# Kernel tuning notes

Measured on AMD Instinct MI355X. Metric: run time of the kernel, lower is better.

## Reference

```python
import jax, jax.numpy as jnp
import numpy as np

DIM = 128
NH = 4
K = 7
PAD = K // 2  # dilation = 1
MLP_HID = 4 * DIM
EPS = 1e-5


def _layernorm(x, w, b):
    m = jnp.mean(x, axis=-1, keepdims=True)
    v = jnp.mean((x - m) ** 2, axis=-1, keepdims=True)
    return (x - m) / jnp.sqrt(v + EPS) * w + b


def _windows(xp, H, W):
    # xp: [B, nh, Hp, Wp, hd] zero-padded; returns [B, nh, H, W, hd, K*K]
    return jnp.stack(
        [xp[:, :, i:i + H, j:j + W, :] for i in range(K) for j in range(K)],
        axis=-1,
    )


def setup_inputs() -> dict:
    key = jax.random.key(0)
    ks = jax.random.split(key, 10)
    s = 0.02
    inp = {
        "x": jax.random.normal(ks[0], (4, 56, 56, DIM), dtype=jnp.float32),
        "ln1_w": jnp.ones((DIM,), jnp.float32),
        "ln1_b": jnp.zeros((DIM,), jnp.float32),
        "w_qkv": jax.random.normal(ks[1], (DIM, 3 * DIM), jnp.float32) * s,
        "b_qkv": jnp.zeros((3 * DIM,), jnp.float32),
        "rpb": jax.random.normal(ks[2], (NH, K * K), jnp.float32) * s,
        "w_proj": jax.random.normal(ks[3], (DIM, DIM), jnp.float32) * s,
        "b_proj": jnp.zeros((DIM,), jnp.float32),
        "ln2_w": jnp.ones((DIM,), jnp.float32),
        "ln2_b": jnp.zeros((DIM,), jnp.float32),
        "w_fc1": jax.random.normal(ks[4], (DIM, MLP_HID), jnp.float32) * s,
        "b_fc1": jnp.zeros((MLP_HID,), jnp.float32),
        "w_fc2": jax.random.normal(ks[5], (MLP_HID, DIM), jnp.float32) * s,
        "b_fc2": jnp.zeros((DIM,), jnp.float32),
    }
    return inp


def _nat_block(x, ln1_w, ln1_b, w_qkv, b_qkv, rpb, w_proj, b_proj,
               ln2_w, ln2_b, w_fc1, b_fc1, w_fc2, b_fc2):
    B, H, W, C = x.shape
    hd = C // NH
    scale = hd ** -0.5

    # --- neighborhood attention ---
    xn = _layernorm(x, ln1_w, ln1_b)
    qkv = xn @ w_qkv + b_qkv                       # [B,H,W,3C]
    qkv = qkv.reshape(B, H, W, 3, NH, hd)
    qkv = jnp.transpose(qkv, (3, 0, 4, 1, 2, 5))   # [3,B,nh,H,W,hd]
    q, k, v = qkv[0] * scale, qkv[1], qkv[2]
    # zero-pad spatial dims (matches F.pad with constant 0 in original)
    pad = ((0, 0), (0, 0), (PAD, PAD), (PAD, PAD), (0, 0))
    kp = jnp.pad(k, pad)
    vp = jnp.pad(v, pad)
    kw = _windows(kp, H, W)                        # [B,nh,H,W,hd,49]
    vw = _windows(vp, H, W)
    attn = jnp.einsum('bnhwd,bnhwdk->bnhwk', q, kw)
    attn = attn + rpb[None, :, None, None, :]
    attn = jax.nn.softmax(attn, axis=-1)
    out = jnp.einsum('bnhwk,bnhwdk->bnhwd', attn, vw)  # [B,nh,H,W,hd]
    out = jnp.transpose(out, (0, 2, 3, 1, 4)).reshape(B, H, W, C)
    x = x + (out @ w_proj + b_proj)

    # --- MLP ---
    xn2 = _layernorm(x, ln2_w, ln2_b)
    h = jax.nn.gelu(xn2 @ w_fc1 + b_fc1, approximate=False)
    x = x + (h @ w_fc2 + b_fc2)
    return x


def reference(x, ln1_w, ln1_b, w_qkv, b_qkv, rpb, w_proj, b_proj,
              ln2_w, ln2_b, w_fc1, b_fc1, w_fc2, b_fc2):
    return _nat_block(x, ln1_w, ln1_b, w_qkv, b_qkv, rpb, w_proj, b_proj,
                      ln2_w, ln2_b, w_fc1, b_fc1, w_fc2, b_fc2)
```

## Files before the change

### kernel.cpp

```cpp
#include <hip/hip_runtime.h>

using bf16x8 = __attribute__((ext_vector_type(8))) short;
using f32x4  = __attribute__((ext_vector_type(4))) float;
typedef unsigned short u16;
typedef __attribute__((ext_vector_type(8))) unsigned short u16x8;
typedef __attribute__((ext_vector_type(4))) unsigned short u16x4;

__device__ __forceinline__ u16 f2b(float f){
  unsigned int i=__float_as_uint(f);
  return (u16)((i + 0x7FFFu + ((i>>16)&1u))>>16);
}
__device__ __forceinline__ float b2f(u16 u){
  union{unsigned int i; float f;}v; v.i=((unsigned int)u)<<16; return v.f;
}
__device__ __forceinline__ void async16(const void* g, void* l){
  __builtin_amdgcn_global_load_lds((__attribute__((address_space(1))) void*)(g),
                                   (__attribute__((address_space(3))) void*)(l), 16, 0, 0);
}
__device__ __forceinline__ float gelu_tanh(float v){
  float u = v*(0.7978845608f + 0.0356774081f*v*v);
  float e = __expf(-2.0f*fabsf(u));
  float th = (1.0f-e)/(1.0f+e);
  th = (u<0.f)? -th : th;
  return 0.5f*v*(1.0f+th);
}

__global__ void prep_kernel(const float* __restrict__ wqkv, const float* __restrict__ wproj,
                            const float* __restrict__ wfc1, const float* __restrict__ wfc2,
                            u16* __restrict__ tqkv, u16* __restrict__ tproj,
                            u16* __restrict__ tfc1, u16* __restrict__ tfc2)
{
  int idx = blockIdx.x*256 + threadIdx.x;
  if (idx < 49152){ int n=idx>>7, k=idx&127; tqkv[idx]=f2b(wqkv[k*384+n]); }
  else if (idx < 65536){ int t=idx-49152; int n=t>>7, k=t&127; tproj[t]=f2b(wproj[k*128+n]); }
  else if (idx < 131072){ int t=idx-65536; int n=t>>7, k=t&127; tfc1[t]=f2b(wfc1[k*512+n]); }
  else if (idx < 196608){ int t=idx-131072; int n=t>>9, k=t&511; tfc2[t]=f2b(wfc2[k*128+n]); }
}

__global__ __launch_bounds__(256)
void qkv_ln_kernel(const float* __restrict__ x,
                   const float* __restrict__ ln1w, const float* __restrict__ ln1b,
                   const u16* __restrict__ tqkv, const float* __restrict__ bqkv,
                   u16* __restrict__ qb, u16* __restrict__ kb, u16* __restrict__ vb)
{
  __shared__ __align__(16) char smem[49152];
  char* lA = smem;
  char* lB = smem + 16384;

  const int tid = threadIdx.x;
  const int lane = tid&63, wid = tid>>6;
  const int quad = lane>>4, lrow = lane&15;
  const int m0 = blockIdx.x*64;
  const int wm = (wid&1)*32, wn = (wid>>1)*64;

  {
    const int row = tid>>2, q = tid&3;
    float xv[32];
    const float4* xr = (const float4*)(x + (size_t)(m0+row)*128 + q*32);
    float s=0.f, sq=0.f;
    #pragma unroll
    for (int c4=0;c4<8;c4++){
      float4 t = xr[c4];
      xv[c4*4]=t.x; xv[c4*4+1]=t.y; xv[c4*4+2]=t.z; xv[c4*4+3]=t.w;
      s += t.x+t.y+t.z+t.w;
      sq += t.x*t.x+t.y*t.y+t.z*t.z+t.w*t.w;
    }
    s  += __shfl_xor(s,1);  s  += __shfl_xor(s,2);
    sq += __shfl_xor(sq,1); sq += __shfl_xor(sq,2);
    float mean = s*0.0078125f;
    float rstd = rsqrtf(sq*0.0078125f - mean*mean + 1e-5f);
    const float4* wr = (const float4*)(ln1w + q*32);
    const float4* br = (const float4*)(ln1b + q*32);
    u16 nv[32];
    #pragma unroll
    for (int c4=0;c4<8;c4++){
      float4 w4 = wr[c4], b4 = br[c4];
      nv[c4*4]   = f2b((xv[c4*4]  -mean)*rstd*w4.x + b4.x);
      nv[c4*4+1] = f2b((xv[c4*4+1]-mean)*rstd*w4.y + b4.y);
      nv[c4*4+2] = f2b((xv[c4*4+2]-mean)*rstd*w4.z + b4.z);
      nv[c4*4+3] = f2b((xv[c4*4+3]-mean)*rstd*w4.w + b4.w);
    }
    #pragma unroll
    for (int cc=0;cc<4;cc++){
      u16x8 pk;
      #pragma unroll
      for (int e=0;e<8;e++) pk[e] = nv[cc*8+e];
      *(u16x8*)(lA + (((q*4+cc)*64 + row)<<4)) = pk;
    }
  }

  for (int nc=0; nc<3; nc++){
    __syncthreads();
    #pragma unroll
    for (int kk=0;kk<8;kk++){
      int i = tid + kk*256;
      int n = i&127, c = i>>7;
      async16(tqkv + (size_t)(nc*128+n)*128 + c*8, lB + i*16);
    }
    __syncthreads();

    f32x4 acc[2][4] = {};
    #pragma unroll
    for (int ks=0;ks<4;ks++){
      bf16x8 af[2], bfr[4];
      #pragma unroll
      for (int i=0;i<2;i++) af[i]  = ((const bf16x8*)lA)[(ks*4+quad)*64  + wm + i*16 + lrow];
      #pragma unroll
      for (int j=0;j<4;j++) bfr[j] = ((const bf16x8*)lB)[(ks*4+quad)*128 + wn + j*16 + lrow];
      #pragma unroll
      for (int i=0;i<2;i++)
        #pragma unroll
        for (int j=0;j<4;j++)
          acc[i][j] = __builtin_amdgcn_mfma_f32_16x16x32_bf16(af[i], bfr[j], acc[i][j], 0,0,0);
    }

    const float scale = 0.17677669529663687f;
    u16* dst = (nc==0)? qb : ((nc==1)? kb : vb);
    #pragma unroll
    for (int j=0;j<4;j++){
      int col = wn + j*16 + lrow;
      float bia = bqkv[nc*128 + col];
      #pragma unroll
      for (int i=0;i<2;i++){
        #pragma unroll
        for (int r=0;r<4;r++){
          int row = m0 + wm + i*16 + quad*4 + r;
          float val = acc[i][j][r] + bia;
          if (nc==0) val *= scale;
          dst[(size_t)row*128 + col] = f2b(val);
        }
      }
    }
  }
}

#define KT_S 40
#define VT_S 232
#define P_S  152
__global__ __launch_bounds__(256)
void attn_kernel(const u16* __restrict__ qb, const u16* __restrict__ kb,
                 const u16* __restrict__ vb, const float* __restrict__ rpb,
                 u16* __restrict__ aout)
{
  __shared__ __align__(16) char smem[50192];
  u16*  kt   = (u16*)smem;
  u16*  vt   = (u16*)(smem + 15680);
  u16*  Pm   = (u16*)(smem + 30528);
  float* srpb= (float*)(smem + 49984);

  const int tid = threadIdx.x;
  const int tile = blockIdx.x, bh = blockIdx.y;
  const int b = bh>>2, h = bh&3;
  const int ty = (tile/7)*8, tx = (tile%7)*8;
  const int lane = tid&63, wid = tid>>6;
  const int quad = lane>>4, lrow = lane&15;

  #pragma unroll
  for (int kk=0;kk<4;kk++){
    int i = tid + kk*256;
    if (i < 784){
      int pos = i>>2, oct = i&3;
      int hy = pos/14, hx = pos - hy*14;
      int gy = ty + hy - 3, gx = tx + hx - 3;
      u16x8 kv = {0,0,0,0,0,0,0,0};
      if (gy>=0 && gy<56 && gx>=0 && gx<56)
        kv = *(const u16x8*)(kb + ((size_t)(b*3136 + gy*56 + gx)*128 + h*32 + oct*8));
      *(u16x8*)(kt + pos*KT_S + oct*8) = kv;
    }
  }
  #pragma unroll
  for (int kk=0;kk<4;kk++){
    int i = tid + kk*256;
    if (i < 896){
      int pos = i>>2, oct = i&3;
      u16x8 vv = {0,0,0,0,0,0,0,0};
      if (pos < 196){
        int hy = pos/14, hx = pos - hy*14;
        int gy = ty + hy - 3, gx = tx + hx - 3;
        if (gy>=0 && gy<56 && gx>=0 && gx<56)
          vv = *(const u16x8*)(vb + ((size_t)(b*3136 + gy*56 + gx)*128 + h*32 + oct*8));
      }
      #pragma unroll
      for (int j=0;j<8;j++) vt[(oct*8+j)*VT_S + pos] = vv[j];
    }
  }
  if (tid < 49) srpb[tid] = rpb[h*49 + tid];
  __syncthreads();

  const int pxq = wid*16 + lrow;
  const int tokq = b*3136 + (ty + (pxq>>3))*56 + tx + (pxq&7);
  bf16x8 qf = *(const bf16x8*)(qb + (size_t)tokq*128 + h*32 + quad*8);

  f32x4 sc[7];
  const f32x4 zf = {0.f,0.f,0.f,0.f};
  #pragma unroll
  for (int cg=0;cg<7;cg++){
    int pos = wid*28 + cg*16 + lrow;
    bf16x8 kf = *(const bf16x8*)(kt + pos*KT_S + quad*8);
    sc[cg] = __builtin_amdgcn_mfma_f32_16x16x32_bf16(qf, kf, zf, 0,0,0);
  }

  const int lyq = quad>>1;
  #pragma unroll
  for (int cg=0;cg<7;cg++){
    int np = cg*16 + lrow;
    int nh = np/14, hx = np - nh*14;
    int dy = nh - lyq;
    #pragma unroll
    for (int r=0;r<4;r++){
      int lx = (quad*4+r)&7;
      int dx = hx - lx;
      bool in = ((unsigned)dy<7u) && ((unsigned)dx<7u);
      float bias = srpb[in ? (dy*7+dx) : 0];
      sc[cg][r] = in ? (sc[cg][r] + bias) : -1e30f;
    }
  }
  float rmax[4], lsum[4], inv[4];
  #pragma unroll
  for (int r=0;r<4;r++){
    float m = sc[0][r];
    #pragma unroll
    for (int cg=1;cg<7;cg++) m = fmaxf(m, sc[cg][r]);
    m = fmaxf(m, __shfl_xor(m,1)); m = fmaxf(m, __shfl_xor(m,2));
    m = fmaxf(m, __shfl_xor(m,4)); m = fmaxf(m, __shfl_xor(m,8));
    rmax[r] = m;
    float l = 0.f;
    #pragma unroll
    for (int cg=0;cg<7;cg++){ float p = __expf(sc[cg][r]-m); sc[cg][r]=p; l+=p; }
    l += __shfl_xor(l,1); l += __shfl_xor(l,2);
    l += __shfl_xor(l,4); l += __shfl_xor(l,8);
    lsum[r]=l; inv[r]=1.f/l;
  }

  u16* Pw = Pm + wid*16*P_S;
  #pragma unroll
  for (int cg=0;cg<7;cg++){
    int np = cg*16 + lrow;
    #pragma unroll
    for (int r=0;r<4;r++)
      Pw[(quad*4+r)*P_S + np] = f2b(sc[cg][r]);
  }
  { int zr = lane>>2, seg = lane&3;
    u16x4 z4 = {0,0,0,0};
    *(u16x4*)(Pw + zr*P_S + 112 + seg*4) = z4; }
  __syncthreads();

  f32x4 oacc[2] = {zf, zf};
  #pragma unroll
  for (int ks=0;ks<4;ks++){
    bf16x8 pf = *(const bf16x8*)(Pw + lrow*P_S + ks*32 + quad*8);
    #pragma unroll
    for (int cg2=0;cg2<2;cg2++){
      bf16x8 vf = *(const bf16x8*)(vt + (cg2*16+lrow)*VT_S + wid*28 + ks*32 + quad*8);
      oacc[cg2] = __builtin_amdgcn_mfma_f32_16x16x32_bf16(pf, vf, oacc[cg2], 0,0,0);
    }
  }
  #pragma unroll
  for (int r=0;r<4;r++){
    int px = wid*16 + quad*4 + r;
    int tok = b*3136 + (ty + (px>>3))*56 + tx + (px&7);
    #pragma unroll
    for (int cg2=0;cg2<2;cg2++){
      int ch = cg2*16 + lrow;
      aout[(size_t)tok*128 + h*32 + ch] = f2b(oacc[cg2][r]*inv[r]);
    }
  }
}

__global__ __launch_bounds__(256)
void mega_mlp_kernel(const u16* __restrict__ aout, const float* __restrict__ x,
                     const u16* __restrict__ tproj, const float* __restrict__ bproj,
                     const float* __restrict__ ln2w, const float* __restrict__ ln2b,
                     const u16* __restrict__ tfc1, const float* __restrict__ bfc1,
                     const u16* __restrict__ tfc2, const float* __restrict__ bfc2,
                     float* __restrict__ out)
{
  __shared__ __align__(16) char smem[65536];
  char* lA  = smem;
  char* lB  = smem + 16384;
  char* xn2 = smem + 49152;

  const int tid = threadIdx.x;
  const int lane = tid&63, wid = tid>>6;
  const int quad = lane>>4, lrow = lane&15;
  const int m0 = blockIdx.x*64;
  const int wm = (wid&1)*32, wn = (wid>>1)*64;
  const int half = wid>>1;

  #pragma unroll
  for (int kk=0;kk<4;kk++){
    int i = tid + kk*256;
    int row = i&63, c = i>>6;
    async16(aout + (size_t)(m0+row)*128 + c*8, lA + i*16);
  }
  #pragma unroll
  for (int kk=0;kk<8;kk++){
    int i = tid + kk*256;
    int n = i&127, c = i>>7;
    async16(tproj + (size_t)n*128 + c*8, lB + i*16);
  }
  __syncthreads();

  f32x4 acc[2][4] = {};
  #pragma unroll
  for (int ks=0;ks<4;ks++){
    bf16x8 af[2], bfr[4];
    #pragma unroll
    for (int i=0;i<2;i++) af[i]  = ((const bf16x8*)lA)[(ks*4+quad)*64  + wm + i*16 + lrow];
    #pragma unroll
    for (int j=0;j<4;j++) bfr[j] = ((const bf16x8*)lB)[(ks*4+quad)*128 + wn + j*16 + lrow];
    #pragma unroll
    for (int i=0;i<2;i++)
      #pragma unroll
      for (int j=0;j<4;j++)
        acc[i][j] = __builtin_amdgcn_mfma_f32_16x16x32_bf16(af[i], bfr[j], acc[i][j], 0,0,0);
  }
  __syncthreads();

  float x1v[2][4][4];
  float ps[2][4] = {}, pq[2][4] = {};
  #pragma unroll
  for (int j=0;j<4;j++){
    int col = wn + j*16 + lrow;
    float bia = bproj[col];
    #pragma unroll
    for (int i=0;i<2;i++){
      #pragma unroll
      for (int r=0;r<4;r++){
        int row = m0 + wm + i*16 + quad*4 + r;
        float val = acc[i][j][r] + bia + x[(size_t)row*128 + col];
        x1v[i][j][r] = val;
        ps[i][r] += val; pq[i][r] += val*val;
      }
    }
  }
  #pragma unroll
  for (int i=0;i<2;i++)
    #pragma unroll
    for (int r=0;r<4;r++){
      #pragma unroll
      for (int off=1; off<16; off<<=1){
        ps[i][r] += __shfl_xor(ps[i][r], off);
        pq[i][r] += __shfl_xor(pq[i][r], off);
      }
    }
  float* redS = (float*)lA;
  float* redQ = redS + 128;
  if (lrow==0){
    #pragma unroll
    for (int i=0;i<2;i++)
      #pragma unroll
      for (int r=0;r<4;r++){
        int row = wm + i*16 + quad*4 + r;
        redS[half*64 + row] = ps[i][r];
        redQ[half*64 + row] = pq[i][r];
      }
  }
  __syncthreads();

  {
    float w2[4], b2[4];
    #pragma unroll
    for (int j=0;j<4;j++){ int col = wn+j*16+lrow; w2[j]=ln2w[col]; b2[j]=ln2b[col]; }
    #pragma unroll
    for (int i=0;i<2;i++){
      #pragma unroll
      for (int r=0;r<4;r++){
        int row = wm + i*16 + quad*4 + r;
        float mean = (redS[row] + redS[64+row])*0.0078125f;
        float var  = (redQ[row] + redQ[64+row])*0.0078125f - mean*mean;
        float rstd = rsqrtf(var + 1e-5f);
        #pragma unroll
        for (int j=0;j<4;j++){
          int col = wn + j*16 + lrow;
          u16 hv = f2b((x1v[i][j][r]-mean)*rstd*w2[j] + b2[j]);
          ((u16*)xn2)[((col>>3)*64 + row)*8 + (col&7)] = hv;
        }
      }
    }
  }
  __syncthreads();

  f32x4 acc3[2][4] = {};
  for (int nc=0; nc<4; nc++){
    if (nc>0) __syncthreads();
    #pragma unroll
    for (int kk=0;kk<8;kk++){
      int i = tid + kk*256;
      int n = i&127, c = i>>7;
      async16(tfc1 + (size_t)(nc*128+n)*128 + c*8, lB + i*16);
    }
    __syncthreads();

    f32x4 acc2[2][4] = {};
    #pragma unroll
    for (int ks=0;ks<4;ks++){
      bf16x8 af[2], bfr[4];
      #pragma unroll
      for (int i=0;i<2;i++) af[i]  = ((const bf16x8*)xn2)[(ks*4+quad)*64  + wm + i*16 + lrow];
      #pragma unroll
      for (int j=0;j<4;j++) bfr[j] = ((const bf16x8*)lB)[(ks*4+quad)*128 + wn + j*16 + lrow];
      #pragma unroll
      for (int i=0;i<2;i++)
        #pragma unroll
        for (int j=0;j<4;j++)
          acc2[i][j] = __builtin_amdgcn_mfma_f32_16x16x32_bf16(af[i], bfr[j], acc2[i][j], 0,0,0);
    }
    #pragma unroll
    for (int j=0;j<4;j++){
      int col = wn + j*16 + lrow;
      float bia = bfc1[nc*128 + col];
      #pragma unroll
      for (int i=0;i<2;i++){
        #pragma unroll
        for (int r=0;r<4;r++){
          int row = wm + i*16 + quad*4 + r;
          float g = gelu_tanh(acc2[i][j][r] + bia);
          ((u16*)lA)[((col>>3)*64 + row)*8 + (col&7)] = f2b(g);
        }
      }
    }
    __syncthreads();
    #pragma unroll
    for (int kk=0;kk<8;kk++){
      int i = tid + kk*256;
      int n = i&127, c = i>>7;
      async16(tfc2 + (size_t)n*512 + nc*128 + c*8, lB + i*16);
    }
    __syncthreads();

    #pragma unroll
    for (int ks=0;ks<4;ks++){
      bf16x8 af[2], bfr[4];
      #pragma unroll
      for (int i=0;i<2;i++) af[i]  = ((const bf16x8*)lA)[(ks*4+quad)*64  + wm + i*16 + lrow];
      #pragma unroll
      for (int j=0;j<4;j++) bfr[j] = ((const bf16x8*)lB)[(ks*4+quad)*128 + wn + j*16 + lrow];
      #pragma unroll
      for (int i=0;i<2;i++)
        #pragma unroll
        for (int j=0;j<4;j++)
          acc3[i][j] = __builtin_amdgcn_mfma_f32_16x16x32_bf16(af[i], bfr[j], acc3[i][j], 0,0,0);
    }
  }

  #pragma unroll
  for (int j=0;j<4;j++){
    int col = wn + j*16 + lrow;
    float bia = bfc2[col];
    #pragma unroll
    for (int i=0;i<2;i++){
      #pragma unroll
      for (int r=0;r<4;r++){
        int row = m0 + wm + i*16 + quad*4 + r;
        out[(size_t)row*128 + col] = acc3[i][j][r] + bia + x1v[i][j][r];
      }
    }
  }
}

extern "C" void kernel_launch(void* const* d_in, const int* in_sizes, int n_in,
                              void* d_out, int out_size, void* d_ws, size_t ws_size,
                              hipStream_t stream)
{
  const float* x     =(const float*)d_in[0];
  const float* ln1w  =(const float*)d_in[1];
  const float* ln1b  =(const float*)d_in[2];
  const float* wqkv  =(const float*)d_in[3];
  const float* bqkv  =(const float*)d_in[4];
  const float* rpb   =(const float*)d_in[5];
  const float* wproj =(const float*)d_in[6];
  const float* bproj =(const float*)d_in[7];
  const float* ln2w  =(const float*)d_in[8];
  const float* ln2b  =(const float*)d_in[9];
  const float* wfc1  =(const float*)d_in[10];
  const float* bfc1  =(const float*)d_in[11];
  const float* wfc2  =(const float*)d_in[12];
  const float* bfc2  =(const float*)d_in[13];

  char* ws=(char*)d_ws;
  size_t o=0;
  u16* tqkv =(u16*)(ws+o); o+=98304;
  u16* tproj=(u16*)(ws+o); o+=32768;
  u16* tfc1 =(u16*)(ws+o); o+=131072;
  u16* tfc2 =(u16*)(ws+o); o+=131072;
  u16* aout =(u16*)(ws+o); o+=3211264;
  u16* qb   =(u16*)(ws+o); o+=3211264;
  u16* kb   =(u16*)(ws+o); o+=3211264;
  u16* vb   =(u16*)(ws+o); o+=3211264;

  prep_kernel<<<768,256,0,stream>>>(wqkv,wproj,wfc1,wfc2,tqkv,tproj,tfc1,tfc2);
  qkv_ln_kernel<<<196,256,0,stream>>>(x,ln1w,ln1b,tqkv,bqkv,qb,kb,vb);
  attn_kernel<<<dim3(49,16),256,0,stream>>>(qb,kb,vb,rpb,aout);
  mega_mlp_kernel<<<196,256,0,stream>>>(aout,x,tproj,bproj,ln2w,ln2b,
                                        tfc1,bfc1,tfc2,bfc2,(float*)d_out);
}
```

Baseline: 142.3 us.

## Halve row tiles and split QKV output chunks across grid to fill more CUs

The QKV+LayerNorm kernel now processes 32 rows per block and assigns each of the three Q/K/V output chunks to a separate blockIdx.y, giving 1176 blocks instead of 196. It also issues the weight load before the LayerNorm so the two overlap. The fused proj+LN2+MLP kernel likewise drops to 32-row tiles (392 blocks) with smaller LDS. The goal is better occupancy on a 256-CU part, at the cost of recomputing LayerNorm three times and reloading weights per block.

```diff
diff --git a/kernel.cpp b/kernel.cpp
--- a/kernel.cpp
+++ b/kernel.cpp
@@ -43,37 +43,45 @@
                    const u16* __restrict__ tqkv, const float* __restrict__ bqkv,
                    u16* __restrict__ qb, u16* __restrict__ kb, u16* __restrict__ vb)
 {
-  __shared__ __align__(16) char smem[49152];
+  __shared__ __align__(16) char smem[40960];
   char* lA = smem;
-  char* lB = smem + 16384;
+  char* lB = smem + 8192;
 
   const int tid = threadIdx.x;
   const int lane = tid&63, wid = tid>>6;
   const int quad = lane>>4, lrow = lane&15;
-  const int m0 = blockIdx.x*64;
-  const int wm = (wid&1)*32, wn = (wid>>1)*64;
+  const int m0 = blockIdx.x*32;
+  const int nc = blockIdx.y;
+  const int wm = (wid&1)*16, wn = (wid>>1)*64;
+
+  #pragma unroll
+  for (int kk=0;kk<8;kk++){
+    int i = tid + kk*256;
+    int n = i&127, c = i>>7;
+    async16(tqkv + (size_t)(nc*128+n)*128 + c*8, lB + i*16);
+  }
 
   {
-    const int row = tid>>2, q = tid&3;
-    float xv[32];
-    const float4* xr = (const float4*)(x + (size_t)(m0+row)*128 + q*32);
+    const int row = tid>>3, g = tid&7;
+    float xv[16];
+    const float4* xr = (const float4*)(x + (size_t)(m0+row)*128 + g*16);
     float s=0.f, sq=0.f;
     #pragma unroll
-    for (int c4=0;c4<8;c4++){
+    for (int c4=0;c4<4;c4++){
       float4 t = xr[c4];
       xv[c4*4]=t.x; xv[c4*4+1]=t.y; xv[c4*4+2]=t.z; xv[c4*4+3]=t.w;
       s += t.x+t.y+t.z+t.w;
       sq += t.x*t.x+t.y*t.y+t.z*t.z+t.w*t.w;
     }
-    s  += __shfl_xor(s,1);  s  += __shfl_xor(s,2);
-    sq += __shfl_xor(sq,1); sq += __shfl_xor(sq,2);
+    s  += __shfl_xor(s,1);  s  += __shfl_xor(s,2);  s  += __shfl_xor(s,4);
+    sq += __shfl_xor(sq,1); sq += __shfl_xor(sq,2); sq += __shfl_xor(sq,4);
     float mean = s*0.0078125f;
     float rstd = rsqrtf(sq*0.0078125f - mean*mean + 1e-5f);
-    const float4* wr = (const float4*)(ln1w + q*32);
-    const float4* br = (const float4*)(ln1b + q*32);
-    u16 nv[32];
-    #pragma unroll
-    for (int c4=0;c4<8;c4++){
+    const float4* wr = (const float4*)(ln1w + g*16);
+    const float4* br = (const float4*)(ln1b + g*16);
+    u16 nv[16];
+    #pragma unroll
+    for (int c4=0;c4<4;c4++){
       float4 w4 = wr[c4], b4 = br[c4];
       nv[c4*4]   = f2b((xv[c4*4]  -mean)*rstd*w4.x + b4.x);
       nv[c4*4+1] = f2b((xv[c4*4+1]-mean)*rstd*w4.y + b4.y);
@@ -81,55 +89,38 @@
       nv[c4*4+3] = f2b((xv[c4*4+3]-mean)*rstd*w4.w + b4.w);
     }
     #pragma unroll
-    for (int cc=0;cc<4;cc++){
+    for (int cc=0;cc<2;cc++){
       u16x8 pk;
       #pragma unroll
       for (int e=0;e<8;e++) pk[e] = nv[cc*8+e];
-      *(u16x8*)(lA + (((q*4+cc)*64 + row)<<4)) = pk;
-    }
-  }
-
-  for (int nc=0; nc<3; nc++){
-    __syncthreads();
-    #pragma unroll
-    for (int kk=0;kk<8;kk++){
-      int i = tid + kk*256;
-      int n = i&127, c = i>>7;
-      async16(tqkv + (size_t)(nc*128+n)*128 + c*8, lB + i*16);
-    }
-    __syncthreads();
-
-    f32x4 acc[2][4] = {};
-    #pragma unroll
-    for (int ks=0;ks<4;ks++){
-      bf16x8 af[2], bfr[4];
-      #pragma unroll
-      for (int i=0;i<2;i++) af[i]  = ((const bf16x8*)lA)[(ks*4+quad)*64  + wm + i*16 + lrow];
-      #pragma unroll
-      for (int j=0;j<4;j++) bfr[j] = ((const bf16x8*)lB)[(ks*4+quad)*128 + wn + j*16 + lrow];
-      #pragma unroll
-      for (int i=0;i<2;i++)
-        #pragma unroll
-        for (int j=0;j<4;j++)
-          acc[i][j] = __builtin_amdgcn_mfma_f32_16x16x32_bf16(af[i], bfr[j], acc[i][j], 0,0,0);
-    }
-
-    const float scale = 0.17677669529663687f;
-    u16* dst = (nc==0)? qb : ((nc==1)? kb : vb);
+      *(u16x8*)(lA + (((g*2+cc)*32 + row)<<4)) = pk;
+    }
+  }
+  __syncthreads();
+
+  f32x4 acc[4] = {};
+  #pragma unroll
+  for (int ks=0;ks<4;ks++){
+    bf16x8 af = ((const bf16x8*)lA)[(ks*4+quad)*32 + wm + lrow];
     #pragma unroll
     for (int j=0;j<4;j++){
-      int col = wn + j*16 + lrow;
-      float bia = bqkv[nc*128 + col];
-      #pragma unroll
-      for (int i=0;i<2;i++){
-        #pragma unroll
-        for (int r=0;r<4;r++){
-          int row = m0 + wm + i*16 + quad*4 + r;
-          float val = acc[i][j][r] + bia;
-          if (nc==0) val *= scale;
-          dst[(size_t)row*128 + col] = f2b(val);
-        }
-      }
+      bf16x8 bfr = ((const bf16x8*)lB)[(ks*4+quad)*128 + wn + j*16 + lrow];
+      acc[j] = __builtin_amdgcn_mfma_f32_16x16x32_bf16(af, bfr, acc[j], 0,0,0);
+    }
+  }
+
+  const float scale = 0.17677669529663687f;
+  u16* dst = (nc==0)? qb : ((nc==1)? kb : vb);
+  #pragma unroll
+  for (int j=0;j<4;j++){
+    int col = wn + j*16 + lrow;
+    float bia = bqkv[nc*128 + col];
+    #pragma unroll
+    for (int r=0;r<4;r++){
+      int row = m0 + wm + quad*4 + r;
+      float val = acc[j][r] + bia;
+      if (nc==0) val *= scale;
+      dst[(size_t)row*128 + col] = f2b(val);
     }
   }
 }
@@ -215,7 +206,7 @@
       sc[cg][r] = in ? (sc[cg][r] + bias) : -1e30f;
     }
   }
-  float rmax[4], lsum[4], inv[4];
+  float inv[4];
   #pragma unroll
   for (int r=0;r<4;r++){
     float m = sc[0][r];
@@ -223,13 +214,12 @@
     for (int cg=1;cg<7;cg++) m = fmaxf(m, sc[cg][r]);
     m = fmaxf(m, __shfl_xor(m,1)); m = fmaxf(m, __shfl_xor(m,2));
     m = fmaxf(m, __shfl_xor(m,4)); m = fmaxf(m, __shfl_xor(m,8));
-    rmax[r] = m;
     float l = 0.f;
     #pragma unroll
     for (int cg=0;cg<7;cg++){ float p = __expf(sc[cg][r]-m); sc[cg][r]=p; l+=p; }
     l += __shfl_xor(l,1); l += __shfl_xor(l,2);
     l += __shfl_xor(l,4); l += __shfl_xor(l,8);
-    lsum[r]=l; inv[r]=1.f/l;
+    inv[r]=1.f/l;
   }
 
   u16* Pw = Pm + wid*16*P_S;
@@ -275,22 +265,24 @@
                      const u16* __restrict__ tfc2, const float* __restrict__ bfc2,
                      float* __restrict__ out)
 {
-  __shared__ __align__(16) char smem[65536];
+  __shared__ __align__(16) char smem[49664];
   char* lA  = smem;
-  char* lB  = smem + 16384;
-  char* xn2 = smem + 49152;
+  char* lB  = smem + 8192;
+  char* xn2 = smem + 40960;
+  float* redS = (float*)(smem + 49152);
+  float* redQ = redS + 64;
 
   const int tid = threadIdx.x;
   const int lane = tid&63, wid = tid>>6;
   const int quad = lane>>4, lrow = lane&15;
-  const int m0 = blockIdx.x*64;
-  const int wm = (wid&1)*32, wn = (wid>>1)*64;
+  const int m0 = blockIdx.x*32;
+  const int wm = (wid&1)*16, wn = (wid>>1)*64;
   const int half = wid>>1;
 
   #pragma unroll
-  for (int kk=0;kk<4;kk++){
+  for (int kk=0;kk<2;kk++){
     int i = tid + kk*256;
-    int row = i&63, c = i>>6;
+    int row = i&31, c = i>>5;
     async16(aout + (size_t)(m0+row)*128 + c*8, lA + i*16);
   }
   #pragma unroll
@@ -301,60 +293,46 @@
   }
   __syncthreads();
 
-  f32x4 acc[2][4] = {};
+  f32x4 acc[4] = {};
   #pragma unroll
   for (int ks=0;ks<4;ks++){
-    bf16x8 af[2], bfr[4];
-    #pragma unroll
-    for (int i=0;i<2;i++) af[i]  = ((const bf16x8*)lA)[(ks*4+quad)*64  + wm + i*16 + lrow];
-    #pragma unroll
-    for (int j=0;j<4;j++) bfr[j] = ((const bf16x8*)lB)[(ks*4+quad)*128 + wn + j*16 + lrow];
-    #pragma unroll
-    for (int i=0;i<2;i++)
-      #pragma unroll
-      for (int j=0;j<4;j++)
-        acc[i][j] = __builtin_amdgcn_mfma_f32_16x16x32_bf16(af[i], bfr[j], acc[i][j], 0,0,0);
-  }
-  __syncthreads();
-
-  float x1v[2][4][4];
-  float ps[2][4] = {}, pq[2][4] = {};
+    bf16x8 af = ((const bf16x8*)lA)[(ks*4+quad)*32 + wm + lrow];
+    #pragma unroll
+    for (int j=0;j<4;j++){
+      bf16x8 bfr = ((const bf16x8*)lB)[(ks*4+quad)*128 + wn + j*16 + lrow];
+      acc[j] = __builtin_amdgcn_mfma_f32_16x16x32_bf16(af, bfr, acc[j], 0,0,0);
+    }
+  }
+
+  float x1v[4][4];
+  float ps[4] = {}, pq[4] = {};
   #pragma unroll
   for (int j=0;j<4;j++){
     int col = wn + j*16 + lrow;
     float bia = bproj[col];
     #pragma unroll
-    for (int i=0;i<2;i++){
-      #pragma unroll
-      for (int r=0;r<4;r++){
-        int row = m0 + wm + i*16 + quad*4 + r;
-        float val = acc[i][j][r] + bia + x[(size_t)row*128 + col];
-        x1v[i][j][r] = val;
-        ps[i][r] += val; pq[i][r] += val*val;
-      }
-    }
-  }
-  #pragma unroll
-  for (int i=0;i<2;i++)
-    #pragma unroll
-    for (int r=0;r<4;r++){
-      #pragma unroll
-      for (int off=1; off<16; off<<=1){
-        ps[i][r] += __shfl_xor(ps[i][r], off);
-        pq[i][r] += __shfl_xor(pq[i][r], off);
-      }
-    }
-  float* redS = (float*)lA;
-  float* redQ = redS + 128;
+    for (int r=0;r<4;r++){
+      int row = m0 + wm + quad*4 + r;
+      float val = acc[j][r] + bia + x[(size_t)row*128 + col];
+      x1v[j][r] = val;
+      ps[r] += val; pq[r] += val*val;
+    }
+  }
+  #pragma unroll
+  for (int r=0;r<4;r++){
+    #pragma unroll
+    for (int off=1; off<16; off<<=1){
+      ps[r] += __shfl_xor(ps[r], off);
+      pq[r] += __shfl_xor(pq[r], off);
+    }
+  }
   if (lrow==0){
     #pragma unroll
-    for (int i=0;i<2;i++)
-      #pragma unroll
-      for (int r=0;r<4;r++){
-        int row = wm + i*16 + quad*4 + r;
-        redS[half*64 + row] = ps[i][r];
-        redQ[half*64 + row] = pq[i][r];
-      }
+    for (int r=0;r<4;r++){
+      int row = wm + quad*4 + r;
+      redS[half*32 + row] = ps[r];
+      redQ[half*32 + row] = pq[r];
+    }
   }
   __syncthreads();
 
@@ -363,25 +341,22 @@
     #pragma unroll
     for (int j=0;j<4;j++){ int col = wn+j*16+lrow; w2[j]=ln2w[col]; b2[j]=ln2b[col]; }
     #pragma unroll
-    for (int i=0;i<2;i++){
-      #pragma unroll
-      for (int r=0;r<4;r++){
-        int row = wm + i*16 + quad*4 + r;
-        float mean = (redS[row] + redS[64+row])*0.0078125f;
-        float var  = (redQ[row] + redQ[64+row])*0.0078125f - mean*mean;
-        float rstd = rsqrtf(var + 1e-5f);
-        #pragma unroll
-        for (int j=0;j<4;j++){
-          int col = wn + j*16 + lrow;
-          u16 hv = f2b((x1v[i][j][r]-mean)*rstd*w2[j] + b2[j]);
-          ((u16*)xn2)[((col>>3)*64 + row)*8 + (col&7)] = hv;
-        }
+    for (int r=0;r<4;r++){
+      int row = wm + quad*4 + r;
+      float mean = (redS[row] + redS[32+row])*0.0078125f;
+      float var  = (redQ[row] + redQ[32+row])*0.0078125f - mean*mean;
+      float rstd = rsqrtf(var + 1e-5f);
+      #pragma unroll
+      for (int j=0;j<4;j++){
+        int col = wn + j*16 + lrow;
+        u16 hv = f2b((x1v[j][r]-mean)*rstd*w2[j] + b2[j]);
+        ((u16*)xn2)[((col>>3)*32 + row)*8 + (col&7)] = hv;
       }
     }
   }
   __syncthreads();
 
-  f32x4 acc3[2][4] = {};
+  f32x4 acc3[4] = {};
   for (int nc=0; nc<4; nc++){
     if (nc>0) __syncthreads();
     #pragma unroll
@@ -392,32 +367,25 @@
     }
     __syncthreads();
 
-    f32x4 acc2[2][4] = {};
+    f32x4 acc2[4] = {};
     #pragma unroll
     for (int ks=0;ks<4;ks++){
-      bf16x8 af[2], bfr[4];
-      #pragma unroll
-      for (int i=0;i<2;i++) af[i]  = ((const bf16x8*)xn2)[(ks*4+quad)*64  + wm + i*16 + lrow];
-      #pragma unroll
-      for (int j=0;j<4;j++) bfr[j] = ((const bf16x8*)lB)[(ks*4+quad)*128 + wn + j*16 + lrow];
-      #pragma unroll
-      for (int i=0;i<2;i++)
-        #pragma unroll
-        for (int j=0;j<4;j++)
-          acc2[i][j] = __builtin_amdgcn_mfma_f32_16x16x32_bf16(af[i], bfr[j], acc2[i][j], 0,0,0);
+      bf16x8 af = ((const bf16x8*)xn2)[(ks*4+quad)*32 + wm + lrow];
+      #pragma unroll
+      for (int j=0;j<4;j++){
+        bf16x8 bfr = ((const bf16x8*)lB)[(ks*4+quad)*128 + wn + j*16 + lrow];
+        acc2[j] = __builtin_amdgcn_mfma_f32_16x16x32_bf16(af, bfr, acc2[j], 0,0,0);
+      }
     }
     #pragma unroll
     for (int j=0;j<4;j++){
       int col = wn + j*16 + lrow;
       float bia = bfc1[nc*128 + col];
       #pragma unroll
-      for (int i=0;i<2;i++){
-        #pragma unroll
-        for (int r=0;r<4;r++){
-          int row = wm + i*16 + quad*4 + r;
-          float g = gelu_tanh(acc2[i][j][r] + bia);
-          ((u16*)lA)[((col>>3)*64 + row)*8 + (col&7)] = f2b(g);
-        }
+      for (int r=0;r<4;r++){
+        int row = wm + quad*4 + r;
+        float g = gelu_tanh(acc2[j][r] + bia);
+        ((u16*)lA)[((col>>3)*32 + row)*8 + (col&7)] = f2b(g);
       }
     }
     __syncthreads();
@@ -431,16 +399,12 @@
 
     #pragma unroll
     for (int ks=0;ks<4;ks++){
-      bf16x8 af[2], bfr[4];
-      #pragma unroll
-      for (int i=0;i<2;i++) af[i]  = ((const bf16x8*)lA)[(ks*4+quad)*64  + wm + i*16 + lrow];
-      #pragma unroll
-      for (int j=0;j<4;j++) bfr[j] = ((const bf16x8*)lB)[(ks*4+quad)*128 + wn + j*16 + lrow];
-      #pragma unroll
-      for (int i=0;i<2;i++)
-        #pragma unroll
-        for (int j=0;j<4;j++)
-          acc3[i][j] = __builtin_amdgcn_mfma_f32_16x16x32_bf16(af[i], bfr[j], acc3[i][j], 0,0,0);
+      bf16x8 af = ((const bf16x8*)lA)[(ks*4+quad)*32 + wm + lrow];
+      #pragma unroll
+      for (int j=0;j<4;j++){
+        bf16x8 bfr = ((const bf16x8*)lB)[(ks*4+quad)*128 + wn + j*16 + lrow];
+        acc3[j] = __builtin_amdgcn_mfma_f32_16x16x32_bf16(af, bfr, acc3[j], 0,0,0);
+      }
     }
   }
 
@@ -449,12 +413,9 @@
     int col = wn + j*16 + lrow;
     float bia = bfc2[col];
     #pragma unroll
-    for (int i=0;i<2;i++){
-      #pragma unroll
-      for (int r=0;r<4;r++){
-        int row = m0 + wm + i*16 + quad*4 + r;
-        out[(size_t)row*128 + col] = acc3[i][j][r] + bia + x1v[i][j][r];
-      }
+    for (int r=0;r<4;r++){
+      int row = m0 + wm + quad*4 + r;
+      out[(size_t)row*128 + col] = acc3[j][r] + bia + x1v[j][r];
     }
   }
 }
@@ -490,8 +451,8 @@
   u16* vb   =(u16*)(ws+o); o+=3211264;
 
   prep_kernel<<<768,256,0,stream>>>(wqkv,wproj,wfc1,wfc2,tqkv,tproj,tfc1,tfc2);
-  qkv_ln_kernel<<<196,256,0,stream>>>(x,ln1w,ln1b,tqkv,bqkv,qb,kb,vb);
+  qkv_ln_kernel<<<dim3(392,3),256,0,stream>>>(x,ln1w,ln1b,tqkv,bqkv,qb,kb,vb);
   attn_kernel<<<dim3(49,16),256,0,stream>>>(qb,kb,vb,rpb,aout);
-  mega_mlp_kernel<<<196,256,0,stream>>>(aout,x,tproj,bproj,ln2w,ln2b,
+  mega_mlp_kernel<<<392,256,0,stream>>>(aout,x,tproj,bproj,ln2w,ln2b,
                                         tfc1,bfc1,tfc2,bfc2,(float*)d_out);
 }
```

New measurement: 140.4 us. Within noise of the previous version (-1.4%).
